# Kernel tuning notes

Measured on AMD Instinct MI355X. Metric: run time of the kernel, lower is better.

The kernel has to match this reference:

```python
import jax, jax.numpy as jnp
import numpy as np

D_MODEL = 2048
SLOTS = 8
D_FIELD = 256  # SLOTS * D_FIELD == proj output dim == 2048
BATCH = 2
SEQ = 4096


def setup_inputs() -> dict:
    key = jax.random.key(0)
    k1, k2 = jax.random.split(key, 2)
    x = jax.random.normal(k1, (BATCH, SEQ, D_MODEL), dtype=jnp.float32)
    # nn.Linear(d_model, slots*d_field): weight [out, in], bias [out]
    W = jax.random.normal(k2, (SLOTS * D_FIELD, D_MODEL), dtype=jnp.float32) * (1.0 / np.sqrt(D_MODEL))
    b = jnp.zeros((SLOTS * D_FIELD,), dtype=jnp.float32)
    horizons = jnp.array([1., 2., 4., 8., 16., 32., 64., 128.], dtype=jnp.float32)
    alphas = jnp.exp(-1.0 / horizons)  # per-slot EMA decay, length SLOTS
    return {"x": x, "W": W, "b": b, "alphas": alphas}


def reference(x, W, b, alphas):
    B, S, _ = x.shape
    # projection: [B,S,d_model] @ [d_model, slots*d_field] -> [B,S,slots,d_field]
    updates = (jnp.einsum('bsd,od->bso', x, W) + b).reshape(B, S, SLOTS, D_FIELD)
    # linear recurrence state_t = alpha * state_{t-1} + u_t, state_0 = 0,
    # via log-depth associative scan with elements (a_t, u_t)
    a = jnp.broadcast_to(alphas[None, None, :, None], updates.shape)

    def combine(c1, c2):
        a1, u1 = c1
        a2, u2 = c2
        return (a1 * a2, a2 * u1 + u2)

    _, state = jax.lax.associative_scan(combine, (a, updates), axis=1)
    return state  # [B,S,slots,d_field]
```

## Files before the change

kernel.cpp:

```cpp
#include <hip/hip_runtime.h>
#include <hip/hip_bf16.h>
#include <stdint.h>
#include <stddef.h>

#define D_MODEL 2048
#define NOUT    2048
#define BATCH   2
#define SEQ     4096
#define M_TOTAL (BATCH*SEQ)
#define SLOTS   8
#define D_FIELD 256
#define CHUNK   32
#define NCHUNK  (SEQ/CHUNK)
#define NWAVEC  64

typedef __attribute__((ext_vector_type(4))) float  floatx4;
typedef __attribute__((ext_vector_type(8))) __bf16 bf16x8;
typedef __attribute__((ext_vector_type(4))) __bf16 bf16x4;

__device__ __forceinline__ void async_copy16(const void* gsrc, void* ldst) {
  __builtin_amdgcn_global_load_lds(
      (__attribute__((address_space(1))) const void*)(uintptr_t)gsrc,
      (__attribute__((address_space(3))) void*)(uintptr_t)ldst,
      16, 0, 0);
}

__global__ void cast_kernel(const float* __restrict__ x,
                            const float* __restrict__ W,
                            __bf16* __restrict__ xb,
                            __bf16* __restrict__ wb,
                            int* __restrict__ ctr) {
  if (blockIdx.x == 0 && threadIdx.x < 8)
    __hip_atomic_store(&ctr[threadIdx.x], 0, __ATOMIC_RELAXED, __HIP_MEMORY_SCOPE_AGENT);
  const long long nx = (long long)M_TOTAL * D_MODEL;
  const long long nw = (long long)NOUT * D_MODEL;
  long long base = ((long long)blockIdx.x * blockDim.x + threadIdx.x) * 4;
  if (base < nx) {
    float4 v = *(const float4*)(x + base);
    bf16x4 o;
    o[0] = (__bf16)v.x; o[1] = (__bf16)v.y; o[2] = (__bf16)v.z; o[3] = (__bf16)v.w;
    *(bf16x4*)(xb + base) = o;
  } else {
    long long j = base - nx;
    if (j < nw) {
      float4 v = *(const float4*)(W + j);
      bf16x4 o;
      o[0] = (__bf16)v.x; o[1] = (__bf16)v.y; o[2] = (__bf16)v.z; o[3] = (__bf16)v.w;
      *(bf16x4*)(wb + j) = o;
    }
  }
}

#define VMW4 asm volatile("s_waitcnt vmcnt(4)" ::: "memory")
#define VMW2 asm volatile("s_waitcnt vmcnt(2)" ::: "memory")
#define VMW0 asm volatile("s_waitcnt vmcnt(0)" ::: "memory")
#define BAR  __builtin_amdgcn_s_barrier()

#define DSRD(off) (*(const bf16x8*)(smem + (off)))

#define STG(GP, ROFF, DSTOFF, KTN) do{ \
  async_copy16((GP) + (ROFF) + (KTN)*64,      smem + (DSTOFF)); \
  async_copy16((GP) + (ROFF) + (KTN)*64 + 32, smem + (DSTOFF) + 1024); }while(0)

#define RD_AF(BUF, MOFF) do{ \
  _Pragma("unroll") for (int i_ = 0; i_ < 4; ++i_){ \
  _Pragma("unroll") for (int k_ = 0; k_ < 2; ++k_){ \
    afr[i_][k_] = DSRD((BUF)*32768 + ((wM8+(MOFF)+i_)*2+k_)*1024 + fragOff); }} }while(0)

#define RD_BF(BUF, NOFF, DST) do{ \
  _Pragma("unroll") for (int j_ = 0; j_ < 2; ++j_){ \
  _Pragma("unroll") for (int k_ = 0; k_ < 2; ++k_){ \
    DST[j_][k_] = DSRD(65536 + (BUF)*32768 + ((wN4+(NOFF)+j_)*2+k_)*1024 + fragOff); }} }while(0)

#define MFMA_Q(AM, AN, BFR) do{ \
  __builtin_amdgcn_s_setprio(1); \
  _Pragma("unroll") for (int i_ = 0; i_ < 4; ++i_){ \
  _Pragma("unroll") for (int j_ = 0; j_ < 2; ++j_){ \
  _Pragma("unroll") for (int k_ = 0; k_ < 2; ++k_){ \
    acc[(AM)+i_][(AN)+j_] = __builtin_amdgcn_mfma_f32_16x16x32_bf16( \
        afr[i_][k_], BFR[j_][k_], acc[(AM)+i_][(AN)+j_], 0, 0, 0); }}} \
  __builtin_amdgcn_s_setprio(0); }while(0)

#define KTILE(BUF, KTN, DO_STG) do{ \
   \
  RD_AF(BUF, 0); \
  RD_BF(BUF, 0, bfr0); \
  if (DO_STG) STG(gA, rA0, ((BUF)^1)*32768 + dA0, KTN); \
  if (DO_STG) { VMW4; } else { VMW2; } \
  BAR; \
  MFMA_Q(0, 0, bfr0); \
   \
  RD_BF(BUF, 2, bfr1); \
  if (DO_STG) STG(gB, rB0, ((BUF)^1)*32768 + dB0, KTN); \
  if (DO_STG) { VMW4; } else { VMW0; } \
  BAR; \
  MFMA_Q(0, 2, bfr1); \
   \
  RD_AF(BUF, 4); \
  if (DO_STG) STG(gB, rB1, ((BUF)^1)*32768 + dB1, KTN); \
  BAR; \
  MFMA_Q(4, 2, bfr1); \
   \
  if (DO_STG) { STG(gA, rA1, ((BUF)^1)*32768 + dA1, KTN); VMW4; } \
  BAR; \
  MFMA_Q(4, 0, bfr0); \
}while(0)

#define CARRY_LD(P) __hip_atomic_load((P), __ATOMIC_RELAXED, __HIP_MEMORY_SCOPE_AGENT)

__global__ __launch_bounds__(512, 2) void gemm_scan_kernel(
    const __bf16* __restrict__ A,
    const __bf16* __restrict__ Bw,
    const float*  __restrict__ bias,
    const float*  __restrict__ alphas,
    float* __restrict__ C,
    float* __restrict__ wc,
    int*   __restrict__ ctr) {
  extern __shared__ __align__(16) char smem[];
  const int t    = threadIdx.x;
  const int lane = t & 63;
  const int w    = t >> 6;
  const int wM   = w >> 2;
  const int wN   = w & 3;
  const int m0   = blockIdx.x * 256;
  const int n0   = blockIdx.y * 256;

  const int lq = lane >> 4, lr = lane & 15;
  const int fragOff = (lr*64 + lq*16) ^ (((lr >> 3) & 1) << 5);
  const int wM8 = wM*8, wN4 = wN*4;

  const int lrow = lane >> 2;
  const int lcol = ((lane & 3) * 8) ^ ((lane >> 5) * 16);
  const int srA0 = (w & 3) + ((w >> 2) << 3), srA1 = srA0 + 4;
  const int srB0 = (w & 1) + ((w >> 1) << 2), srB1 = srB0 + 2;
  const __bf16* gA = A  + (size_t)m0 * D_MODEL + lcol;
  const __bf16* gB = Bw + (size_t)n0 * D_MODEL + lcol;
  const int rA0 = (srA0*16 + lrow) * D_MODEL;
  const int rA1 = (srA1*16 + lrow) * D_MODEL;
  const int rB0 = (srB0*16 + lrow) * D_MODEL;
  const int rB1 = (srB1*16 + lrow) * D_MODEL;
  const int dA0 = srA0*2048 + lane*16;
  const int dA1 = srA1*2048 + lane*16;
  const int dB0 = 65536 + srB0*2048 + lane*16;
  const int dB1 = 65536 + srB1*2048 + lane*16;

  floatx4 acc[8][4] = {};
  bf16x8 afr[4][2], bfr0[2][2], bfr1[2][2];

  STG(gA, rA0, dA0, 0);
  STG(gB, rB0, dB0, 0);
  STG(gB, rB1, dB1, 0);
  STG(gA, rA1, dA1, 0);
  VMW4;
  BAR;

#pragma unroll 1
  for (int p = 0; p < 15; ++p) {
    KTILE(0, 2*p+1, true);
    KTILE(1, 2*p+2, true);
  }
  KTILE(0, 31, true);
  KTILE(1, 0, false);

  const int mW0 = m0 + wM*128;
  const int nW0 = n0 + wN*64;
  const float alpha = alphas[nW0 >> 8];
  const float a2 = alpha*alpha, a4 = a2*a2, a8 = a4*a4, a16 = a8*a8, a32 = a16*a16;
  const float a64 = a32*a32, a128 = a64*a64;
  const float a256 = a128*a128, a512 = a256*a256, a1024 = a512*a512;
  float aq = 1.f;
#pragma unroll
  for (int i = 0; i < 3; ++i) if (i < 3 - lq) aq *= a4;
  float a4p = 1.f;
#pragma unroll
  for (int i = 0; i < 3; ++i) if (i < lq) a4p *= a4;
  const int bb  = mW0 >> 12;
  const int j0w = (mW0 & (SEQ - 1)) >> 5;
  const int jw  = j0w >> 2;
  float* wcb = wc + (size_t)bb * NWAVEC * NOUT;

  float bvv[4], tmv[4][8], rcl[4][4];
#pragma unroll
  for (int nf = 0; nf < 4; ++nf) {
    const int n = nW0 + nf*16 + lr;
    bvv[nf] = bias[n];
    const float bv = bvv[nf];
#pragma unroll
    for (int mf = 0; mf < 8; ++mf) {
      const floatx4 av = acc[mf][nf];
      tmv[nf][mf] = (((av[0]+bv)*alpha + (av[1]+bv))*alpha + (av[2]+bv))*alpha + (av[3]+bv);
    }
#pragma unroll
    for (int c = 0; c < 4; ++c) {
      float s = (tmv[nf][2*c]*a16 + tmv[nf][2*c+1]) * aq;
      s += __shfl_xor(s, 16, 64);
      s += __shfl_xor(s, 32, 64);
      rcl[nf][c] = s;
    }
    const float Wv = ((rcl[nf][0]*a32 + rcl[nf][1])*a32 + rcl[nf][2])*a32 + rcl[nf][3];
    if (lq == 0)
      __hip_atomic_store(&wcb[(size_t)jw*NOUT + n], Wv,
                         __ATOMIC_RELAXED, __HIP_MEMORY_SCOPE_AGENT);
  }

  __syncthreads();
  if (t == 0) {
    __hip_atomic_fetch_add(&ctr[blockIdx.y], 1, __ATOMIC_ACQ_REL, __HIP_MEMORY_SCOPE_AGENT);
    while (__hip_atomic_load(&ctr[blockIdx.y], __ATOMIC_ACQUIRE, __HIP_MEMORY_SCOPE_AGENT) < 32)
      __builtin_amdgcn_s_sleep(2);
  }
  __syncthreads();

  {
    const float* wcl = wcb + (nW0 + lq*16 + lr);
    float H = 0.f;
    int jp = 0;
    for (; jp + 8 <= jw; jp += 8) {
      float v[8];
#pragma unroll
      for (int i = 0; i < 8; ++i)
        v[i] = CARRY_LD(&wcl[(size_t)(jp + i)*NOUT]);
      float h = v[0];
#pragma unroll
      for (int i = 1; i < 8; ++i) h = h*a128 + v[i];
      H = H*a1024 + h;
    }
    for (; jp < jw; ++jp)
      H = H*a128 + CARRY_LD(&wcl[(size_t)jp*NOUT]);

    float s0[4];
#pragma unroll
    for (int nf = 0; nf < 4; ++nf) s0[nf] = __shfl(H, nf*16 + lr, 64);

#pragma unroll
    for (int nf = 0; nf < 4; ++nf) {
      const int n = nW0 + nf*16 + lr;
      const float bv = bvv[nf];
      float sp = s0[nf];
#pragma unroll
      for (int c = 0; c < 4; ++c) {
        if (c > 0)
          sp = a32*sp + rcl[nf][c-1];
        float ulo[4], uhi[4];
#pragma unroll
        for (int i = 0; i < 4; ++i) {
          ulo[i] = acc[2*c][nf][i]   + bv;
          uhi[i] = acc[2*c+1][nf][i] + bv;
        }
        const float Tlo = tmv[nf][2*c];
        const float Thi = tmv[nf][2*c+1];
        const float t0  = __shfl(Tlo, lr,      64);
        const float t1  = __shfl(Tlo, 16 + lr, 64);
        const float t2  = __shfl(Tlo, 32 + lr, 64);
        const float t3  = __shfl(Tlo, 48 + lr, 64);
        const float th0 = __shfl(Thi, lr,      64);
        const float th1 = __shfl(Thi, 16 + lr, 64);
        const float th2 = __shfl(Thi, 32 + lr, 64);
        float h = 0.f;
        if (lq > 0) h = t0;
        if (lq > 1) h = h*a4 + t1;
        if (lq > 2) h = h*a4 + t2;
        float Slo = a4p*sp + h;
        const float smid = (((t0*a4 + t1)*a4 + t2)*a4 + t3) + a16*sp;
        float hh = 0.f;
        if (lq > 0) hh = th0;
        if (lq > 1) hh = hh*a4 + th1;
        if (lq > 2) hh = hh*a4 + th2;
        float Shi = a4p*smid + hh;
        const size_t rowb = (size_t)(mW0 + 2*c*16 + lq*4);
        float s = Slo;
#pragma unroll
        for (int i = 0; i < 4; ++i) { s = alpha*s + ulo[i]; C[(rowb + i)*NOUT + n] = s; }
        s = Shi;
#pragma unroll
        for (int i = 0; i < 4; ++i) { s = alpha*s + uhi[i]; C[(rowb + 16 + i)*NOUT + n] = s; }
      }
    }
  }
}

extern "C" void kernel_launch(void* const* d_in, const int* in_sizes, int n_in,
                              void* d_out, int out_size, void* d_ws, size_t ws_size,
                              hipStream_t stream) {
  const float* x      = (const float*)d_in[0];
  const float* W      = (const float*)d_in[1];
  const float* bias   = (const float*)d_in[2];
  const float* alphas = (const float*)d_in[3];
  float* out = (float*)d_out;

  __bf16* xb = (__bf16*)d_ws;
  __bf16* wb = (__bf16*)((char*)d_ws + (size_t)M_TOTAL * D_MODEL * 2);
  float* wc  = (float*)((char*)d_ws + (size_t)M_TOTAL * D_MODEL * 2
                                     + (size_t)NOUT * D_MODEL * 2);
  int* ctr   = (int*)((char*)d_ws + (size_t)M_TOTAL * D_MODEL * 2
                                   + (size_t)NOUT * D_MODEL * 2
                                   + (size_t)BATCH * NWAVEC * NOUT * 4);

  {
    const long long total = ((long long)M_TOTAL * D_MODEL + (long long)NOUT * D_MODEL) / 4;
    const int blocks = (int)((total + 255) / 256);
    cast_kernel<<<blocks, 256, 0, stream>>>(x, W, xb, wb, ctr);
  }
  {
    dim3 grid(M_TOTAL / 256, NOUT / 256);
    gemm_scan_kernel<<<grid, 512, 131072, stream>>>(xb, wb, bias, alphas, out, wc, ctr);
  }
}
```

Measured before the change: 199.3 us.

## Fuse x fp32-to-bf16 cast into GEMM A-tile loading

Result: slower. 238.3 us (+19.6%).

```diff
diff --git a/kernel.cpp b/kernel.cpp
--- a/kernel.cpp
+++ b/kernel.cpp
@@ -25,42 +25,44 @@
       16, 0, 0);
 }
 
-__global__ void cast_kernel(const float* __restrict__ x,
-                            const float* __restrict__ W,
-                            __bf16* __restrict__ xb,
+__global__ void cast_kernel(const float* __restrict__ W,
                             __bf16* __restrict__ wb,
                             int* __restrict__ ctr) {
   if (blockIdx.x == 0 && threadIdx.x < 8)
     __hip_atomic_store(&ctr[threadIdx.x], 0, __ATOMIC_RELAXED, __HIP_MEMORY_SCOPE_AGENT);
-  const long long nx = (long long)M_TOTAL * D_MODEL;
   const long long nw = (long long)NOUT * D_MODEL;
-  long long base = ((long long)blockIdx.x * blockDim.x + threadIdx.x) * 4;
-  if (base < nx) {
-    float4 v = *(const float4*)(x + base);
+  long long j = ((long long)blockIdx.x * blockDim.x + threadIdx.x) * 4;
+  if (j < nw) {
+    float4 v = *(const float4*)(W + j);
     bf16x4 o;
     o[0] = (__bf16)v.x; o[1] = (__bf16)v.y; o[2] = (__bf16)v.z; o[3] = (__bf16)v.w;
-    *(bf16x4*)(xb + base) = o;
-  } else {
-    long long j = base - nx;
-    if (j < nw) {
-      float4 v = *(const float4*)(W + j);
-      bf16x4 o;
-      o[0] = (__bf16)v.x; o[1] = (__bf16)v.y; o[2] = (__bf16)v.z; o[3] = (__bf16)v.w;
-      *(bf16x4*)(wb + j) = o;
-    }
+    *(bf16x4*)(wb + j) = o;
   }
 }
 
-#define VMW4 asm volatile("s_waitcnt vmcnt(4)" ::: "memory")
-#define VMW2 asm volatile("s_waitcnt vmcnt(2)" ::: "memory")
-#define VMW0 asm volatile("s_waitcnt vmcnt(0)" ::: "memory")
 #define BAR  __builtin_amdgcn_s_barrier()
+#define LGKM0 asm volatile("s_waitcnt lgkmcnt(0)" ::: "memory")
 
 #define DSRD(off) (*(const bf16x8*)(smem + (off)))
 
 #define STG(GP, ROFF, DSTOFF, KTN) do{ \
   async_copy16((GP) + (ROFF) + (KTN)*64,      smem + (DSTOFF)); \
   async_copy16((GP) + (ROFF) + (KTN)*64 + 32, smem + (DSTOFF) + 1024); }while(0)
+
+#define LDA_ISSUE(ROFF, KTN) do{ \
+  fA0 = *(const float4*)(gx + (ROFF) + (KTN)*64); \
+  fA1 = *(const float4*)(gx + (ROFF) + (KTN)*64 + 4); \
+  fA2 = *(const float4*)(gx + (ROFF) + (KTN)*64 + 32); \
+  fA3 = *(const float4*)(gx + (ROFF) + (KTN)*64 + 36); }while(0)
+
+#define LDA_COMMIT(DSTOFF) do{ \
+  bf16x8 o0_, o1_; \
+  o0_[0]=(__bf16)fA0.x; o0_[1]=(__bf16)fA0.y; o0_[2]=(__bf16)fA0.z; o0_[3]=(__bf16)fA0.w; \
+  o0_[4]=(__bf16)fA1.x; o0_[5]=(__bf16)fA1.y; o0_[6]=(__bf16)fA1.z; o0_[7]=(__bf16)fA1.w; \
+  o1_[0]=(__bf16)fA2.x; o1_[1]=(__bf16)fA2.y; o1_[2]=(__bf16)fA2.z; o1_[3]=(__bf16)fA2.w; \
+  o1_[4]=(__bf16)fA3.x; o1_[5]=(__bf16)fA3.y; o1_[6]=(__bf16)fA3.z; o1_[7]=(__bf16)fA3.w; \
+  *(bf16x8*)(smem + (DSTOFF)) = o0_; \
+  *(bf16x8*)(smem + (DSTOFF) + 1024) = o1_; }while(0)
 
 #define RD_AF(BUF, MOFF) do{ \
   _Pragma("unroll") for (int i_ = 0; i_ < 4; ++i_){ \
@@ -85,23 +87,23 @@
    \
   RD_AF(BUF, 0); \
   RD_BF(BUF, 0, bfr0); \
-  if (DO_STG) STG(gA, rA0, ((BUF)^1)*32768 + dA0, KTN); \
-  if (DO_STG) { VMW4; } else { VMW2; } \
+  if (DO_STG) { STG(gB, rB0, ((BUF)^1)*32768 + dB0, KTN); LDA_ISSUE(rA0, KTN); } \
   BAR; \
   MFMA_Q(0, 0, bfr0); \
    \
   RD_BF(BUF, 2, bfr1); \
-  if (DO_STG) STG(gB, rB0, ((BUF)^1)*32768 + dB0, KTN); \
-  if (DO_STG) { VMW4; } else { VMW0; } \
+  if (DO_STG) { LDA_COMMIT(((BUF)^1)*32768 + dA0); \
+                STG(gB, rB1, ((BUF)^1)*32768 + dB1, KTN); \
+                LDA_ISSUE(rA1, KTN); } \
   BAR; \
   MFMA_Q(0, 2, bfr1); \
    \
   RD_AF(BUF, 4); \
-  if (DO_STG) STG(gB, rB1, ((BUF)^1)*32768 + dB1, KTN); \
+  if (DO_STG) { LDA_COMMIT(((BUF)^1)*32768 + dA1); } \
   BAR; \
   MFMA_Q(4, 2, bfr1); \
    \
-  if (DO_STG) { STG(gA, rA1, ((BUF)^1)*32768 + dA1, KTN); VMW4; } \
+  if (DO_STG) { LGKM0; } \
   BAR; \
   MFMA_Q(4, 0, bfr0); \
 }while(0)
@@ -109,7 +111,7 @@
 #define CARRY_LD(P) __hip_atomic_load((P), __ATOMIC_RELAXED, __HIP_MEMORY_SCOPE_AGENT)
 
 __global__ __launch_bounds__(512, 2) void gemm_scan_kernel(
-    const __bf16* __restrict__ A,
+    const float*  __restrict__ X,
     const __bf16* __restrict__ Bw,
     const float*  __restrict__ bias,
     const float*  __restrict__ alphas,
@@ -133,7 +135,7 @@
   const int lcol = ((lane & 3) * 8) ^ ((lane >> 5) * 16);
   const int srA0 = (w & 3) + ((w >> 2) << 3), srA1 = srA0 + 4;
   const int srB0 = (w & 1) + ((w >> 1) << 2), srB1 = srB0 + 2;
-  const __bf16* gA = A  + (size_t)m0 * D_MODEL + lcol;
+  const float*  gx = X  + (size_t)m0 * D_MODEL + lcol;
   const __bf16* gB = Bw + (size_t)n0 * D_MODEL + lcol;
   const int rA0 = (srA0*16 + lrow) * D_MODEL;
   const int rA1 = (srA1*16 + lrow) * D_MODEL;
@@ -146,12 +148,15 @@
 
   floatx4 acc[8][4] = {};
   bf16x8 afr[4][2], bfr0[2][2], bfr1[2][2];
-
-  STG(gA, rA0, dA0, 0);
+  float4 fA0, fA1, fA2, fA3;
+
+  LDA_ISSUE(rA0, 0);
   STG(gB, rB0, dB0, 0);
   STG(gB, rB1, dB1, 0);
-  STG(gA, rA1, dA1, 0);
-  VMW4;
+  LDA_COMMIT(dA0);
+  LDA_ISSUE(rA1, 0);
+  LDA_COMMIT(dA1);
+  LGKM0;
   BAR;
 
 #pragma unroll 1
@@ -288,21 +293,18 @@
   const float* alphas = (const float*)d_in[3];
   float* out = (float*)d_out;
 
-  __bf16* xb = (__bf16*)d_ws;
-  __bf16* wb = (__bf16*)((char*)d_ws + (size_t)M_TOTAL * D_MODEL * 2);
-  float* wc  = (float*)((char*)d_ws + (size_t)M_TOTAL * D_MODEL * 2
-                                     + (size_t)NOUT * D_MODEL * 2);
-  int* ctr   = (int*)((char*)d_ws + (size_t)M_TOTAL * D_MODEL * 2
-                                   + (size_t)NOUT * D_MODEL * 2
+  __bf16* wb = (__bf16*)d_ws;
+  float* wc  = (float*)((char*)d_ws + (size_t)NOUT * D_MODEL * 2);
+  int* ctr   = (int*)((char*)d_ws + (size_t)NOUT * D_MODEL * 2
                                    + (size_t)BATCH * NWAVEC * NOUT * 4);
 
   {
-    const long long total = ((long long)M_TOTAL * D_MODEL + (long long)NOUT * D_MODEL) / 4;
+    const long long total = ((long long)NOUT * D_MODEL) / 4;
     const int blocks = (int)((total + 255) / 256);
-    cast_kernel<<<blocks, 256, 0, stream>>>(x, W, xb, wb, ctr);
+    cast_kernel<<<blocks, 256, 0, stream>>>(W, wb, ctr);
   }
   {
     dim3 grid(M_TOTAL / 256, NOUT / 256);
-    gemm_scan_kernel<<<grid, 512, 131072, stream>>>(xb, wb, bias, alphas, out, wc, ctr);
+    gemm_scan_kernel<<<grid, 512, 131072, stream>>>(x, wb, bias, alphas, out, wc, ctr);
   }
 }
```
